# Optimization experiments

Hardware: AMD Instinct MI355X
Metric: run time of the kernel (lower is better)

The kernel has to match this reference:

```python
import jax, jax.numpy as jnp
import numpy as np

BATCH = 524288
TIME_STEPS = 16
LEAK = 0.8
THRESHOLD = 0.5


def spike(m):
    # Hard threshold spike (surrogate gradient only matters for bwd).
    return (m >= THRESHOLD).astype(m.dtype)


def setup_inputs() -> dict:
    key = jax.random.key(0)
    ks = jax.random.split(key, 7)
    return {
        "x": jax.random.normal(ks[0], (BATCH, 2), dtype=jnp.float32),
        "W_ih": jax.random.normal(ks[1], (8, 2), dtype=jnp.float32) * 0.5,
        "b_ih": jax.random.normal(ks[2], (8,), dtype=jnp.float32) * 0.1,
        "W_hh": jax.random.normal(ks[3], (8, 8), dtype=jnp.float32) * 0.5,
        "b_hh": jax.random.normal(ks[4], (8,), dtype=jnp.float32) * 0.1,
        "W_ho": jax.random.normal(ks[5], (1, 8), dtype=jnp.float32) * 0.5,
        "b_ho": jax.random.normal(ks[6], (1,), dtype=jnp.float32) * 0.1,
    }


def reference(x, W_ih, b_ih, W_hh, b_hh, W_ho, b_ho):
    batch = x.shape[0]
    # Input current is identical every step (x is static across time).
    cur1 = x @ W_ih.T + b_ih  # [B, 8]

    def step(carry, _):
        m1, m2, mo, tot = carry
        m1 = LEAK * m1 + cur1
        s1 = spike(m1)
        m1 = m1 * (1.0 - s1)
        m2 = LEAK * m2 + s1 @ W_hh.T + b_hh
        s2 = spike(m2)
        m2 = m2 * (1.0 - s2)
        mo = LEAK * mo + s2 @ W_ho.T + b_ho
        so = spike(mo)
        mo = mo * (1.0 - so)
        return (m1, m2, mo, tot + so), None

    init = (
        jnp.zeros((batch, 8), x.dtype),
        jnp.zeros((batch, 8), x.dtype),
        jnp.zeros((batch, 1), x.dtype),
        jnp.zeros((batch, 1), x.dtype),
    )
    (_, _, _, total), _ = jax.lax.scan(step, init, None, length=TIME_STEPS)
    return total / TIME_STEPS
```

## Files before the change

kernel.cpp:

```cpp
#include <hip/hip_runtime.h>


constexpr bool spikes_by(float c, int p) {
    float m = 0.f;
    for (int t = 0; t < p; ++t) {
        float a = 0.8f * m;
        m = a + c;
        if (m >= 0.5f) return true;
    }
    return false;
}
constexpr unsigned find_B(int p) {
    unsigned lo = 0x3D4CCCCDu;
    unsigned hi = 0x3F19999Au;
    while (hi - lo > 1u) {
        unsigned mid = lo + (hi - lo) / 2u;
        if (spikes_by(__builtin_bit_cast(float, mid), p)) hi = mid;
        else lo = mid;
    }
    return hi;
}
constexpr float kB[17] = {
    0.f,
    __builtin_bit_cast(float, find_B(1)),  __builtin_bit_cast(float, find_B(2)),
    __builtin_bit_cast(float, find_B(3)),  __builtin_bit_cast(float, find_B(4)),
    __builtin_bit_cast(float, find_B(5)),  __builtin_bit_cast(float, find_B(6)),
    __builtin_bit_cast(float, find_B(7)),  __builtin_bit_cast(float, find_B(8)),
    __builtin_bit_cast(float, find_B(9)),  __builtin_bit_cast(float, find_B(10)),
    __builtin_bit_cast(float, find_B(11)), __builtin_bit_cast(float, find_B(12)),
    __builtin_bit_cast(float, find_B(13)), __builtin_bit_cast(float, find_B(14)),
    __builtin_bit_cast(float, find_B(15)), __builtin_bit_cast(float, find_B(16))
};
constexpr unsigned mk_train(int F) {
    unsigned tr = 0;
    if (F <= 16) for (int t = F; t <= 16; t += F) tr |= 1u << (t - 1);
    return tr;
}
constexpr unsigned kTv[18] = {
    0, mk_train(1), mk_train(2),  mk_train(3),  mk_train(4),  mk_train(5),
    mk_train(6),  mk_train(7),  mk_train(8),  mk_train(9),  mk_train(10),
    mk_train(11), mk_train(12), mk_train(13), mk_train(14), mk_train(15),
    mk_train(16), mk_train(17)
};

__device__ __forceinline__ unsigned long long tr8(unsigned long long x) {
    unsigned long long t;
    t = (x ^ (x >> 7))  & 0x00AA00AA00AA00AAull; x = x ^ t ^ (t << 7);
    t = (x ^ (x >> 14)) & 0x0000CCCC0000CCCCull; x = x ^ t ^ (t << 14);
    t = (x ^ (x >> 28)) & 0x00000000F0F0F0F0ull; x = x ^ t ^ (t << 28);
    return x;
}

__global__ __launch_bounds__(256, 8) void snn_kernel(
    const float* __restrict__ x,
    const float* __restrict__ W_ih, const float* __restrict__ b_ih,
    const float* __restrict__ W_hh, const float* __restrict__ b_hh,
    const float* __restrict__ W_ho, const float* __restrict__ b_ho,
    float* __restrict__ out, int n)
{
#pragma clang fp contract(off)
    __shared__ float lut2[256 * 9];
    __shared__ float luto[256];
    __shared__ unsigned Tv[18];

    const int p = threadIdx.x;

    {
        float bits[8];
#pragma unroll
        for (int k = 0; k < 8; ++k) bits[k] = (float)((p >> k) & 1);
#pragma unroll
        for (int j = 0; j < 8; ++j) {
            float acc = 0.f;
#pragma unroll
            for (int k = 0; k < 8; ++k)
                acc = __fmaf_rn(bits[k], W_hh[8 * j + k], acc);
            lut2[p * 9 + j] = acc;
        }
        float acc = 0.f;
#pragma unroll
        for (int k = 0; k < 8; ++k)
            acc = __fmaf_rn(bits[k], W_ho[k], acc);
        luto[p] = acc;
    }
    if (p < 18) Tv[p] = kTv[p];
    __syncthreads();

    const int i = blockIdx.x * 256 + p;
    if (i >= n) return;

    const float2 xv = reinterpret_cast<const float2*>(x)[i];
    float cur[8];
#pragma unroll
    for (int j = 0; j < 8; ++j) {
        float d = __fmaf_rn(xv.y, W_ih[2 * j + 1], __fmul_rn(xv.x, W_ih[2 * j]));
        cur[j] = __fadd_rn(d, b_ih[j]);
    }

    unsigned trn[8];
#pragma unroll
    for (int j = 0; j < 8; ++j) {
        float c = cur[j];
        unsigned cnt = 0;
#pragma unroll
        for (int t = 1; t <= 16; ++t)
            cnt += (c < kB[t]) ? 1u : 0u;
        trn[j] = Tv[cnt + 1u];
    }

    unsigned long long A = 0, A2 = 0;
#pragma unroll
    for (int j = 0; j < 8; ++j) {
        A  |= (unsigned long long)(trn[j] & 0xFFu) << (8 * j);
        A2 |= (unsigned long long)((trn[j] >> 8) & 0xFFu) << (8 * j);
    }
    A = tr8(A); A2 = tr8(A2);

    float bh[8];
#pragma unroll
    for (int j = 0; j < 8; ++j) bh[j] = b_hh[j];
    const float bho = b_ho[0];

    float m2[8] = {0.f,0.f,0.f,0.f,0.f,0.f,0.f,0.f};
    float mo = 0.f, outdot = 0.f;
    unsigned tot = 0;

    float dv[8];
    {
        unsigned b0 = (unsigned)A & 0xFFu;
        A = (A >> 8) | (A2 << 56); A2 >>= 8;
        const float* e0 = &lut2[b0 * 9];
#pragma unroll
        for (int j = 0; j < 8; ++j) dv[j] = e0[j];
    }

#pragma unroll 1
    for (int t = 0; t < 16; ++t) {
        unsigned bN = (unsigned)A & 0xFFu;
        A = (A >> 8) | (A2 << 56); A2 >>= 8;
        unsigned mk2 = 0;
#pragma unroll
        for (int j = 0; j < 8; ++j) {
            float m = __fadd_rn(__fadd_rn(__fmul_rn(0.8f, m2[j]), dv[j]), bh[j]);
            bool s = (m >= 0.5f);
            mk2 |= (s ? 1u : 0u) << j;
            m2[j] = s ? 0.f : m;
        }
        float nO = luto[mk2];
        if (t > 0) {
            float m = __fadd_rn(__fadd_rn(__fmul_rn(0.8f, mo), outdot), bho);
            bool s = (m >= 0.5f);
            tot += s ? 1u : 0u;
            mo = s ? 0.f : m;
        }
        outdot = nO;
        const float* en = &lut2[bN * 9];
#pragma unroll
        for (int j = 0; j < 8; ++j) dv[j] = en[j];
    }
    {
        float m = __fadd_rn(__fadd_rn(__fmul_rn(0.8f, mo), outdot), bho);
        tot += (m >= 0.5f) ? 1u : 0u;
    }

    out[i] = __fmul_rn((float)tot, 0.0625f);
}

extern "C" void kernel_launch(void* const* d_in, const int* in_sizes, int n_in,
                              void* d_out, int out_size, void* d_ws, size_t ws_size,
                              hipStream_t stream) {
    const float* x    = (const float*)d_in[0];
    const float* W_ih = (const float*)d_in[1];
    const float* b_ih = (const float*)d_in[2];
    const float* W_hh = (const float*)d_in[3];
    const float* b_hh = (const float*)d_in[4];
    const float* W_ho = (const float*)d_in[5];
    const float* b_ho = (const float*)d_in[6];
    float* out = (float*)d_out;

    const int n = out_size;
    const int block = 256;
    const int grid = (n + block - 1) / block;
    snn_kernel<<<grid, block, 0, stream>>>(x, W_ih, b_ih, W_hh, b_hh,
                                           W_ho, b_ho, out, n);
}
```

Baseline: 25.23 us.

## Split hidden-layer LUT: half from shared memory, half computed in registers

The shared-memory lookup table for the recurrent layer now covers only the first four hidden neurons, and the output-layer table is dropped. The other four hidden dot products and the output dot product are computed each step with FMAs from weights held in registers. This cuts LDS traffic and bank pressure and shrinks shared memory per block, which may allow more blocks per CU. The cost is extra ALU work and register pressure per step, and the output-layer pipelining (outdot delayed by one step) is removed.

```diff
diff --git a/kernel.cpp b/kernel.cpp
--- a/kernel.cpp
+++ b/kernel.cpp
@@ -59,8 +59,7 @@
     float* __restrict__ out, int n)
 {
 #pragma clang fp contract(off)
-    __shared__ float lut2[256 * 9];
-    __shared__ float luto[256];
+    __shared__ float lut4[256 * 5];
     __shared__ unsigned Tv[18];
 
     const int p = threadIdx.x;
@@ -70,24 +69,33 @@
 #pragma unroll
         for (int k = 0; k < 8; ++k) bits[k] = (float)((p >> k) & 1);
 #pragma unroll
-        for (int j = 0; j < 8; ++j) {
+        for (int j = 0; j < 4; ++j) {
             float acc = 0.f;
 #pragma unroll
             for (int k = 0; k < 8; ++k)
                 acc = __fmaf_rn(bits[k], W_hh[8 * j + k], acc);
-            lut2[p * 9 + j] = acc;
-        }
-        float acc = 0.f;
-#pragma unroll
-        for (int k = 0; k < 8; ++k)
-            acc = __fmaf_rn(bits[k], W_ho[k], acc);
-        luto[p] = acc;
+            lut4[p * 5 + j] = acc;
+        }
     }
     if (p < 18) Tv[p] = kTv[p];
     __syncthreads();
 
     const int i = blockIdx.x * 256 + p;
     if (i >= n) return;
+
+    float whi[4][8];
+#pragma unroll
+    for (int j = 0; j < 4; ++j)
+#pragma unroll
+        for (int k = 0; k < 8; ++k)
+            whi[j][k] = W_hh[8 * (4 + j) + k];
+    float wo[8];
+#pragma unroll
+    for (int k = 0; k < 8; ++k) wo[k] = W_ho[k];
+    float bh[8];
+#pragma unroll
+    for (int j = 0; j < 8; ++j) bh[j] = b_hh[j];
+    const float bho = b_ho[0];
 
     const float2 xv = reinterpret_cast<const float2*>(x)[i];
     float cur[8];
@@ -116,51 +124,65 @@
     }
     A = tr8(A); A2 = tr8(A2);
 
-    float bh[8];
-#pragma unroll
-    for (int j = 0; j < 8; ++j) bh[j] = b_hh[j];
-    const float bho = b_ho[0];
-
     float m2[8] = {0.f,0.f,0.f,0.f,0.f,0.f,0.f,0.f};
-    float mo = 0.f, outdot = 0.f;
+    float mo = 0.f;
     unsigned tot = 0;
 
-    float dv[8];
+    float dvL[4];
+    unsigned bC;
     {
-        unsigned b0 = (unsigned)A & 0xFFu;
+        bC = (unsigned)A & 0xFFu;
         A = (A >> 8) | (A2 << 56); A2 >>= 8;
-        const float* e0 = &lut2[b0 * 9];
-#pragma unroll
-        for (int j = 0; j < 8; ++j) dv[j] = e0[j];
+        const float* e0 = &lut4[bC * 5];
+#pragma unroll
+        for (int j = 0; j < 4; ++j) dvL[j] = e0[j];
     }
 
 #pragma unroll 1
     for (int t = 0; t < 16; ++t) {
         unsigned bN = (unsigned)A & 0xFFu;
         A = (A >> 8) | (A2 << 56); A2 >>= 8;
-        unsigned mk2 = 0;
+
+        float bf[8];
+#pragma unroll
+        for (int k = 0; k < 8; ++k) bf[k] = (float)((bC >> k) & 1u);
+
+        float dvH[4];
+#pragma unroll
+        for (int j = 0; j < 4; ++j) {
+            float acc = 0.f;
+#pragma unroll
+            for (int k = 0; k < 8; ++k)
+                acc = __fmaf_rn(bf[k], whi[j][k], acc);
+            dvH[j] = acc;
+        }
+
+        float bf2[8];
 #pragma unroll
         for (int j = 0; j < 8; ++j) {
-            float m = __fadd_rn(__fadd_rn(__fmul_rn(0.8f, m2[j]), dv[j]), bh[j]);
+            float dv = (j < 4) ? dvL[j] : dvH[j - 4];
+            float m = __fadd_rn(__fadd_rn(__fmul_rn(0.8f, m2[j]), dv), bh[j]);
             bool s = (m >= 0.5f);
-            mk2 |= (s ? 1u : 0u) << j;
+            bf2[j] = s ? 1.0f : 0.0f;
             m2[j] = s ? 0.f : m;
         }
-        float nO = luto[mk2];
-        if (t > 0) {
-            float m = __fadd_rn(__fadd_rn(__fmul_rn(0.8f, mo), outdot), bho);
+
+        float od = 0.f;
+#pragma unroll
+        for (int k = 0; k < 8; ++k)
+            od = __fmaf_rn(bf2[k], wo[k], od);
+
+        {
+            float m = __fadd_rn(__fadd_rn(__fmul_rn(0.8f, mo), od), bho);
             bool s = (m >= 0.5f);
             tot += s ? 1u : 0u;
             mo = s ? 0.f : m;
         }
-        outdot = nO;
-        const float* en = &lut2[bN * 9];
-#pragma unroll
-        for (int j = 0; j < 8; ++j) dv[j] = en[j];
-    }
-    {
-        float m = __fadd_rn(__fadd_rn(__fmul_rn(0.8f, mo), outdot), bho);
-        tot += (m >= 0.5f) ? 1u : 0u;
+
+        const float* en = &lut4[bN * 5];
+#pragma unroll
+        for (int j = 0; j < 4; ++j) dvL[j] = en[j];
+        bC = bN;
     }
 
     out[i] = __fmul_rn((float)tot, 0.0625f);
```

New measurement: 32.68 us. +29.5%, slower.
